# Performance work log

Hardware: AMD Instinct MI355X
Metric: run time of the kernel (lower is better)

Reference implementation:

```python
import jax, jax.numpy as jnp
import numpy as np

THRESHOLD = 0.5
EPS = 1e-6


def setup_inputs() -> dict:
    key = jax.random.key(0)
    k1, k2, k3 = jax.random.split(key, 3)
    B, C, T = 32, 6, 64
    K, N = 8, 128
    S, P = 32, 64
    points = jax.random.normal(k1, (B, C, T, 2), dtype=jnp.float32)
    road_boundary = jax.random.normal(k2, (B, K, N, 2), dtype=jnp.float32)
    centerlines = jax.random.normal(k3, (B, S, P, 2), dtype=jnp.float32)
    return {"points": points, "road_boundary": road_boundary, "centerlines": centerlines}


def _cross(v1, v2):
    return v1[..., 0] * v2[..., 1] - v1[..., 1] * v2[..., 0]


def reference(points, road_boundary, centerlines):
    B, C, T, _ = points.shape
    _, K, N, _ = road_boundary.shape
    _, S, P, _ = centerlines.shape

    # --- min distance to boundary segments ---
    seg_a = road_boundary[:, :, :-1, :]          # (B,K,N-1,2)
    seg_d = road_boundary[:, :, 1:, :] - seg_a   # (B,K,N-1,2)

    p = points[:, None, :, :, None, :]           # (B,1,C,T,1,2)
    a = seg_a[:, :, None, None, :, :]            # (B,K,1,1,N-1,2)
    d = seg_d[:, :, None, None, :, :]            # (B,K,1,1,N-1,2)

    v1 = p - a                                   # (B,K,C,T,N-1,2)
    dot = (v1 * d).sum(-1)                       # (B,K,C,T,N-1)
    edge_sq = (d * d).sum(-1)                    # (B,K,1,1,N-1)
    proj = jnp.clip(dot / (edge_sq + EPS), 0.0, 1.0)
    closest = a + d * proj[..., None]            # (B,K,C,T,N-1,2)
    dist = jnp.sqrt(((p - closest) ** 2).sum(-1))  # (B,K,C,T,N-1)
    min_dist = dist.min(axis=-1).min(axis=1)     # (B,C,T)

    # --- nearest centerline point ---
    cl = centerlines.reshape(B, S * P, 2)        # (B,SP,2)
    v2 = points[:, None, :, :, :] - cl[:, :, None, None, :]  # (B,SP,C,T,2)
    cl_dist_sq = (v2 ** 2).sum(-1)               # (B,SP,C,T)
    idx = jnp.argmin(cl_dist_sq, axis=1)         # (B,C,T)
    closest_cl = cl[jnp.arange(B)[:, None, None], idx]  # (B,C,T,2)

    # --- segment intersection test: (point -> nearest centerline pt) vs boundary edges ---
    a1 = points[:, None, None, :, :, :]          # (B,1,1,C,T,2)
    a2 = closest_cl[:, None, None, :, :, :]      # (B,1,1,C,T,2)
    b1 = seg_a[:, :, :, None, None, :]           # (B,K,N-1,1,1,2)
    db = seg_d[:, :, :, None, None, :]           # (B,K,N-1,1,1,2)

    da = a2 - a1
    dp = a1 - b1                                 # (B,K,N-1,C,T,2)
    dadb = _cross(da, db)                        # (B,K,N-1,C,T)
    t = _cross(da, dp) / (dadb + EPS)
    u = _cross(db, dp) / (dadb + EPS)
    intersect = (t >= 0.0) & (t <= 1.0) & (u >= 0.0) & (u <= 1.0)

    inside = ~jnp.any(intersect, axis=(1, 2))    # (B,C,T)
    min_dist = jnp.where(inside, -min_dist, min_dist)
    return jax.nn.relu(min_dist + THRESHOLD).sum(-1)  # (B,C)
```

## Files before the change

kernel.cpp:

```cpp
#include <hip/hip_runtime.h>

constexpr int cB = 32, cC = 6, cT = 64;
constexpr int cK = 8, cN = 128;
constexpr int cS = 32, cP = 64;
constexpr int NSEG_PAD = cK * cN;
constexpr int NCL  = cS * cP;
constexpr int G = 4;
constexpr int PPW = 4;
constexpr int NIT = NSEG_PAD / 64;
constexpr float F_EPS = 1e-6f;
constexpr float F_THRESHOLD = 0.5f;

__global__ __launch_bounds__(256) void offroad_kernel(
    const float* __restrict__ points,
    const float* __restrict__ road_boundary,
    const float* __restrict__ centerlines,
    float* __restrict__ out)
{
    const int blk  = blockIdx.x;
    const int g    = blk & (G - 1);
    const int bc   = blk >> 2;
    const int b    = bc / cC;
    const int lane = threadIdx.x & 63;
    const int wave = threadIdx.x >> 6;

    const float2* __restrict__ rb2 =
        (const float2*)(road_boundary + (size_t)b * cK * cN * 2);
    const float4* __restrict__ cl4 =
        (const float4*)(centerlines + (size_t)b * NCL * 2);

    const int t0 = (g << 4) | (wave << 2);
    const float* pb = points + (((size_t)bc) * cT + t0) * 2;
    float px[PPW], py[PPW];
    #pragma unroll
    for (int p = 0; p < PPW; ++p) { px[p] = pb[2 * p]; py[p] = pb[2 * p + 1]; }

    float best_d2[PPW];
    int   best_i[PPW];
    #pragma unroll
    for (int p = 0; p < PPW; ++p) { best_d2[p] = 3.4e38f; best_i[p] = 0x7fffffff; }

    {
        int s = lane;
        float4 cp = cl4[s];
        #pragma unroll 4
        for (int i = 0; i < NIT; ++i) {
            const float4 cpc = cp;
            const int sc = s;
            s += 64;
            if (i < NIT - 1) cp = cl4[s];
            const int ia = 2 * sc;
            #pragma unroll
            for (int p = 0; p < PPW; ++p) {
                float dxa = px[p] - cpc.x, dya = py[p] - cpc.y;
                float d2a = dxa * dxa + dya * dya;
                float dxb = px[p] - cpc.z, dyb = py[p] - cpc.w;
                float d2b = dxb * dxb + dyb * dyb;
                float dmin = d2a; int imin = ia;
                if (d2b < d2a) { dmin = d2b; imin = ia + 1; }
                if (dmin < best_d2[p] ||
                    (dmin == best_d2[p] && imin < best_i[p])) {
                    best_d2[p] = dmin; best_i[p] = imin;
                }
            }
        }
    }
    #pragma unroll
    for (int off = 1; off <= 32; off <<= 1) {
        #pragma unroll
        for (int p = 0; p < PPW; ++p) {
            float od2 = __shfl_xor(best_d2[p], off);
            int   oi  = __shfl_xor(best_i[p], off);
            if (od2 < best_d2[p] || (od2 == best_d2[p] && oi < best_i[p])) {
                best_d2[p] = od2; best_i[p] = oi;
            }
        }
    }
    const float2* __restrict__ cl2 = (const float2*)cl4;
    float dax[PPW], day[PPW];
    #pragma unroll
    for (int p = 0; p < PPW; ++p) {
        float2 cc = cl2[best_i[p]];
        dax[p] = cc.x - px[p]; day[p] = cc.y - py[p];
    }

    float min_d2[PPW];
    int   hit[PPW];
    #pragma unroll
    for (int p = 0; p < PPW; ++p) { min_d2[p] = 3.4e38f; hit[p] = 0; }

    {
        int s = lane;
        float2 a = rb2[s];
        #pragma unroll 2
        for (int i = 0; i < NIT; ++i) {
            const float2 ac = a;
            s += 64;
            float2 an = ac;
            if (i < NIT - 1) an = rb2[s];

            float sd_x = __shfl_down(ac.x, 1);
            float sd_y = __shfl_down(ac.y, 1);
            float b0x  = __shfl(an.x, 0);
            float b0y  = __shfl(an.y, 0);
            const bool last = (lane == 63);
            const bool odd  = (i & 1) != 0;
            float nx_x = last ? (odd ? ac.x : b0x) : sd_x;
            float nx_y = last ? (odd ? ac.y : b0y) : sd_y;
            const int valid = (last && odd) ? 0 : 1;

            a = an;

            const float dx = nx_x - ac.x, dy = nx_y - ac.y;
            const float inv_e2 =
                __builtin_amdgcn_rcpf(dx * dx + dy * dy + F_EPS);

            #pragma unroll
            for (int p = 0; p < PPW; ++p) {
                float v1x = px[p] - ac.x, v1y = py[p] - ac.y;
                float proj = (v1x * dx + v1y * dy) * inv_e2;
                proj = __builtin_amdgcn_fmed3f(proj, 0.0f, 1.0f);
                float ex = v1x - dx * proj;
                float ey = v1y - dy * proj;
                min_d2[p] = fminf(min_d2[p], ex * ex + ey * ey);
                float w  = dax[p] * dy - day[p] * dx + F_EPS;
                float w2 = w * w;
                float ct = (dax[p] * v1y - day[p] * v1x) * w;
                float cu = (dx * v1y - dy * v1x) * w;
                bool inb = (ct >= 0.0f) & (ct <= w2) & (cu >= 0.0f) & (cu <= w2);
                hit[p] |= valid & (int)inb;
            }
        }
    }

    #pragma unroll
    for (int off = 1; off <= 32; off <<= 1) {
        #pragma unroll
        for (int p = 0; p < PPW; ++p) {
            min_d2[p] = fminf(min_d2[p], __shfl_xor(min_d2[p], off));
            hit[p]   |= __shfl_xor(hit[p], off);
        }
    }

    float total = 0.0f;
    #pragma unroll
    for (int p = 0; p < PPW; ++p) {
        float md = sqrtf(min_d2[p]);
        float sd = hit[p] ? md : -md;
        total += fmaxf(sd + F_THRESHOLD, 0.0f);
    }
    if (lane == 0)
        atomicAdd(&out[bc], total);
}

extern "C" void kernel_launch(void* const* d_in, const int* in_sizes, int n_in,
                              void* d_out, int out_size, void* d_ws, size_t ws_size,
                              hipStream_t stream) {
    const float* points      = (const float*)d_in[0];
    const float* boundary    = (const float*)d_in[1];
    const float* centerlines = (const float*)d_in[2];
    float* out = (float*)d_out;
    hipMemsetAsync(out, 0, (size_t)out_size * sizeof(float), stream);
    offroad_kernel<<<cB * cC * G, 256, 0, stream>>>(points, boundary, centerlines, out);
}
```

Baseline: 82.17 us.

## Process eight points per wave and load segment endpoints directly instead of shuffling

```diff
diff --git a/kernel.cpp b/kernel.cpp
--- a/kernel.cpp
+++ b/kernel.cpp
@@ -3,15 +3,14 @@
 constexpr int cB = 32, cC = 6, cT = 64;
 constexpr int cK = 8, cN = 128;
 constexpr int cS = 32, cP = 64;
-constexpr int NSEG_PAD = cK * cN;
-constexpr int NCL  = cS * cP;
+constexpr int NCL = cS * cP;
 constexpr int G = 4;
-constexpr int PPW = 4;
-constexpr int NIT = NSEG_PAD / 64;
+constexpr int PPW = 8;
+constexpr int NIT = 16;
 constexpr float F_EPS = 1e-6f;
 constexpr float F_THRESHOLD = 0.5f;
 
-__global__ __launch_bounds__(256) void offroad_kernel(
+__global__ __launch_bounds__(128) void offroad_kernel(
     const float* __restrict__ points,
     const float* __restrict__ road_boundary,
     const float* __restrict__ centerlines,
@@ -28,8 +27,9 @@
         (const float2*)(road_boundary + (size_t)b * cK * cN * 2);
     const float4* __restrict__ cl4 =
         (const float4*)(centerlines + (size_t)b * NCL * 2);
+    const float2* __restrict__ cl2 = (const float2*)cl4;
 
-    const int t0 = (g << 4) | (wave << 2);
+    const int t0 = (g << 4) | (wave << 3);
     const float* pb = points + (((size_t)bc) * cT + t0) * 2;
     float px[PPW], py[PPW];
     #pragma unroll
@@ -76,7 +76,6 @@
             }
         }
     }
-    const float2* __restrict__ cl2 = (const float2*)cl4;
     float dax[PPW], day[PPW];
     #pragma unroll
     for (int p = 0; p < PPW; ++p) {
@@ -89,47 +88,30 @@
     #pragma unroll
     for (int p = 0; p < PPW; ++p) { min_d2[p] = 3.4e38f; hit[p] = 0; }
 
-    {
-        int s = lane;
-        float2 a = rb2[s];
-        #pragma unroll 2
-        for (int i = 0; i < NIT; ++i) {
-            const float2 ac = a;
-            s += 64;
-            float2 an = ac;
-            if (i < NIT - 1) an = rb2[s];
+    #pragma unroll
+    for (int i = 0; i < NIT; ++i) {
+        const int s = lane + 64 * i;
+        const int valid = ((s & (cN - 1)) < cN - 1) ? 1 : 0;
+        const float2 a = rb2[s];
+        const float2 e = rb2[s + valid];
+        const float dx = e.x - a.x, dy = e.y - a.y;
+        const float inv_e2 =
+            __builtin_amdgcn_rcpf(dx * dx + dy * dy + F_EPS);
 
-            float sd_x = __shfl_down(ac.x, 1);
-            float sd_y = __shfl_down(ac.y, 1);
-            float b0x  = __shfl(an.x, 0);
-            float b0y  = __shfl(an.y, 0);
-            const bool last = (lane == 63);
-            const bool odd  = (i & 1) != 0;
-            float nx_x = last ? (odd ? ac.x : b0x) : sd_x;
-            float nx_y = last ? (odd ? ac.y : b0y) : sd_y;
-            const int valid = (last && odd) ? 0 : 1;
-
-            a = an;
-
-            const float dx = nx_x - ac.x, dy = nx_y - ac.y;
-            const float inv_e2 =
-                __builtin_amdgcn_rcpf(dx * dx + dy * dy + F_EPS);
-
-            #pragma unroll
-            for (int p = 0; p < PPW; ++p) {
-                float v1x = px[p] - ac.x, v1y = py[p] - ac.y;
-                float proj = (v1x * dx + v1y * dy) * inv_e2;
-                proj = __builtin_amdgcn_fmed3f(proj, 0.0f, 1.0f);
-                float ex = v1x - dx * proj;
-                float ey = v1y - dy * proj;
-                min_d2[p] = fminf(min_d2[p], ex * ex + ey * ey);
-                float w  = dax[p] * dy - day[p] * dx + F_EPS;
-                float w2 = w * w;
-                float ct = (dax[p] * v1y - day[p] * v1x) * w;
-                float cu = (dx * v1y - dy * v1x) * w;
-                bool inb = (ct >= 0.0f) & (ct <= w2) & (cu >= 0.0f) & (cu <= w2);
-                hit[p] |= valid & (int)inb;
-            }
+        #pragma unroll
+        for (int p = 0; p < PPW; ++p) {
+            float v1x = px[p] - a.x, v1y = py[p] - a.y;
+            float proj = (v1x * dx + v1y * dy) * inv_e2;
+            proj = __builtin_amdgcn_fmed3f(proj, 0.0f, 1.0f);
+            float ex = v1x - dx * proj;
+            float ey = v1y - dy * proj;
+            min_d2[p] = fminf(min_d2[p], ex * ex + ey * ey);
+            float w  = dax[p] * dy - day[p] * dx + F_EPS;
+            float w2 = w * w;
+            float ct = (dax[p] * v1y - day[p] * v1x) * w;
+            float cu = (dx * v1y - dy * v1x) * w;
+            bool inb = (ct >= 0.0f) & (ct <= w2) & (cu >= 0.0f) & (cu <= w2);
+            hit[p] |= valid & (int)inb;
         }
     }
 
@@ -161,5 +143,5 @@
     const float* centerlines = (const float*)d_in[2];
     float* out = (float*)d_out;
     hipMemsetAsync(out, 0, (size_t)out_size * sizeof(float), stream);
-    offroad_kernel<<<cB * cC * G, 256, 0, stream>>>(points, boundary, centerlines, out);
+    offroad_kernel<<<cB * cC * G, 128, 0, stream>>>(points, boundary, centerlines, out);
 }
```

After: 104.8 us. +27.5%, slower.
